# Kernel optimization log

Measured on AMD Instinct MI355X. Metric: run time of the kernel, lower is better.

Reference implementation:

```python
import jax, jax.numpy as jnp
import numpy as np

B, S, H = 1, 2048, 4096
NH = 32
NOPE, ROPE, VD = 128, 64, 128
QHD = NOPE + ROPE          # 192
QLR, KVLR = 1536, 512
BASE = 10000.0
EPS = 1e-6
SCALE = QHD ** -0.5


def _rmsnorm(x, w):
    xf = x.astype(jnp.float32)
    var = jnp.mean(xf * xf, axis=-1, keepdims=True)
    return (w * (xf * jax.lax.rsqrt(var + EPS))).astype(x.dtype)


def _rope_tables(seq_len):
    inv_freq = 1.0 / (BASE ** (jnp.arange(0, ROPE, 2, dtype=jnp.float32) / ROPE))
    t = jnp.arange(seq_len, dtype=jnp.float32)
    freqs = jnp.outer(t, inv_freq)                     # [S, ROPE/2]
    emb = jnp.concatenate([freqs, freqs], axis=-1)     # [S, ROPE]
    return jnp.cos(emb), jnp.sin(emb)


def _rotate_half(x):
    d = x.shape[-1] // 2
    return jnp.concatenate([-x[..., d:], x[..., :d]], axis=-1)


def setup_inputs() -> dict:
    key = jax.random.key(0)
    ks = jax.random.split(key, 8)
    w = 0.02
    hidden_states = jax.random.normal(ks[0], (B, S, H), dtype=jnp.float32)
    # additive causal mask, 0 on/below diagonal, -1e9 above
    causal = jnp.tril(jnp.ones((S, S), dtype=bool))
    attention_mask = jnp.where(causal, 0.0, -1e9).astype(jnp.float32)[None, None]
    return {
        "hidden_states": hidden_states,
        "attention_mask": attention_mask,
        "Wqa": jax.random.normal(ks[1], (QLR, H), dtype=jnp.float32) * w,
        "qa_ln_w": jnp.ones((QLR,), dtype=jnp.float32),
        "Wqb": jax.random.normal(ks[2], (NH * QHD, QLR), dtype=jnp.float32) * w,
        "Wkva": jax.random.normal(ks[3], (KVLR + ROPE, H), dtype=jnp.float32) * w,
        "kva_ln_w": jnp.ones((KVLR,), dtype=jnp.float32),
        "Wkvb": jax.random.normal(ks[4], (NH * (NOPE + VD), KVLR), dtype=jnp.float32) * w,
        "Wo": jax.random.normal(ks[5], (H, NH * VD), dtype=jnp.float32) * w,
    }


def reference(hidden_states, attention_mask, Wqa, qa_ln_w, Wqb, Wkva, kva_ln_w, Wkvb, Wo):
    bsz, q_len, _ = hidden_states.shape
    # --- Q path: low-rank down-proj + RMSNorm + up-proj ---
    q = _rmsnorm(hidden_states @ Wqa.T, qa_ln_w) @ Wqb.T          # [B,S,NH*QHD]
    q = q.reshape(bsz, q_len, NH, QHD).transpose(0, 2, 1, 3)      # [B,NH,S,QHD]
    q_nope, q_pe = q[..., :NOPE], q[..., NOPE:]
    # --- KV path: shared low-rank compression + decoupled rope key ---
    ckv = hidden_states @ Wkva.T                                   # [B,S,KVLR+ROPE]
    compressed_kv, k_pe = ckv[..., :KVLR], ckv[..., KVLR:]
    k_pe = k_pe.reshape(bsz, q_len, 1, ROPE).transpose(0, 2, 1, 3)  # [B,1,S,ROPE]
    kv = _rmsnorm(compressed_kv, kva_ln_w) @ Wkvb.T                # [B,S,NH*(NOPE+VD)]
    kv = kv.reshape(bsz, q_len, NH, NOPE + VD).transpose(0, 2, 1, 3)
    k_nope, value_states = kv[..., :NOPE], kv[..., NOPE:]
    # --- RoPE on decoupled dims ---
    cos, sin = _rope_tables(q_len)                                 # [S,ROPE] broadcast over B,NH
    q_pe = q_pe * cos + _rotate_half(q_pe) * sin
    k_pe = k_pe * cos + _rotate_half(k_pe) * sin
    query_states = jnp.concatenate([q_nope, q_pe], axis=-1)        # [B,NH,S,QHD]
    key_states = jnp.concatenate(
        [k_nope, jnp.broadcast_to(k_pe, (bsz, NH, q_len, ROPE))], axis=-1)
    # --- SDPA ---
    attn = jnp.einsum('bhqd,bhkd->bhqk', query_states, key_states) * SCALE
    attn = attn + attention_mask
    attn = jax.nn.softmax(attn.astype(jnp.float32), axis=-1).astype(query_states.dtype)
    out = jnp.einsum('bhqk,bhkd->bhqd', attn, value_states)        # [B,NH,S,VD]
    out = out.transpose(0, 2, 1, 3).reshape(bsz, q_len, NH * VD)
    return out @ Wo.T
```

## Files before the change

kernel.cpp:

```cpp
#include <hip/hip_runtime.h>

typedef __bf16 bf16;
typedef __bf16 bf16x8 __attribute__((ext_vector_type(8)));
typedef __bf16 bf16x4 __attribute__((ext_vector_type(4)));
typedef float  f32x4  __attribute__((ext_vector_type(4)));

#define NH_    32
#define S_     2048
#define H_     4096
#define NOPE_  128
#define ROPE_  64
#define VD_    128
#define QHD_   192
#define QLR_   1536
#define KVLR_  512
#define QKVA_N 2176

#define MFMA16(a, b, c) __builtin_amdgcn_mfma_f32_16x16x32_bf16(a, b, c, 0, 0, 0)

__device__ __forceinline__ void async_lds16(void* lds, const void* g) {
  __builtin_amdgcn_global_load_lds(
      (const __attribute__((address_space(1))) void*)g,
      (__attribute__((address_space(3))) void*)lds,
      16, 0, 0);
}

#define CVN1 2097152LL
#define CVN2 1572864LL
#define CVN3 655360LL
#define CVN4 2359296LL
#define CVN5 1048576LL
#define CVN6 4194304LL
#define CVC1 (CVN1)
#define CVC2 (CVC1 + CVN2)
#define CVC3 (CVC2 + CVN3)
#define CVC4 (CVC3 + CVN4)
#define CVC5 (CVC4 + CVN5)
#define CVC6 (CVC5 + CVN6)

__device__ __forceinline__ void cv4(const float* __restrict__ s, bf16* __restrict__ d,
                                    long long i) {
  float4 v = ((const float4*)s)[i];
  bf16x4 o;
  o[0] = (bf16)v.x; o[1] = (bf16)v.y; o[2] = (bf16)v.z; o[3] = (bf16)v.w;
  ((bf16x4*)d)[i] = o;
}

__global__ __launch_bounds__(256) void convert_all_kernel(
    const float* __restrict__ hs, const float* __restrict__ Wqa,
    const float* __restrict__ Wkva, const float* __restrict__ Wqb,
    const float* __restrict__ Wkvb, const float* __restrict__ Wo,
    bf16* __restrict__ hidden_bf, bf16* __restrict__ qkva_w,
    bf16* __restrict__ Wqb_bf, bf16* __restrict__ Wkvb_bf,
    bf16* __restrict__ Wo_bf) {
  long long i = (long long)blockIdx.x * 256 + threadIdx.x;
  const long long stride = (long long)gridDim.x * 256;
  for (; i < CVC6; i += stride) {
    if (i < CVC1) {
      cv4(hs, hidden_bf, i);
    } else if (i < CVC2) {
      cv4(Wqa, qkva_w, i - CVC1);
    } else if (i < CVC3) {
      long long j = i - CVC2;
      long long r = j >> 10;
      bf16x4 o;
      if (r < 576) {
        float4 v = ((const float4*)Wkva)[j];
        o[0] = (bf16)v.x; o[1] = (bf16)v.y; o[2] = (bf16)v.z; o[3] = (bf16)v.w;
      } else {
        o[0] = o[1] = o[2] = o[3] = (bf16)0.f;
      }
      ((bf16x4*)(qkva_w + (size_t)QLR_ * H_))[j] = o;
    } else if (i < CVC4) {
      cv4(Wqb, Wqb_bf, i - CVC3);
    } else if (i < CVC5) {
      cv4(Wkvb, Wkvb_bf, i - CVC4);
    } else {
      cv4(Wo, Wo_bf, i - CVC5);
    }
  }
}

__global__ __launch_bounds__(256) void rope_tables_kernel(float* __restrict__ ct,
                                                          float* __restrict__ st) {
  int i = blockIdx.x * 256 + threadIdx.x;
  int t = i >> 5, f = i & 31;
  float inv = powf(10000.0f, -(float)f / 32.0f);
  float ang = (float)t * inv;
  ct[i] = cosf(ang);
  st[i] = sinf(ang);
}

__global__ __launch_bounds__(256) void rope_q_kernel(bf16* __restrict__ qb,
                                                     const float* __restrict__ ct,
                                                     const float* __restrict__ st) {
  int i = blockIdx.x * 256 + threadIdx.x;
  int t = i >> 10;
  int rem = i & 1023;
  int h = rem >> 5, j = rem & 31;
  size_t base = (size_t)t * (NH_ * QHD_) + h * QHD_ + NOPE_;
  float a = (float)qb[base + j], b = (float)qb[base + 32 + j];
  float c = ct[t * 32 + j], s = st[t * 32 + j];
  qb[base + j]      = (bf16)(a * c - b * s);
  qb[base + 32 + j] = (bf16)(b * c + a * s);
}

__global__ __launch_bounds__(256) void rope_k_kernel(const float* __restrict__ part,
                                                     const float* __restrict__ ct,
                                                     const float* __restrict__ st,
                                                     bf16* __restrict__ kpe,
                                                     long long pstr) {
  int i = blockIdx.x * 256 + threadIdx.x;
  int t = i >> 5, j = i & 31;
  size_t base = (size_t)t * QKVA_N + 2048;
  float a = part[base + j] + part[base + j + pstr];
  float b = part[base + 32 + j] + part[base + 32 + j + pstr];
  float c = ct[i], s = st[i];
  kpe[t * 64 + j]      = (bf16)(a * c - b * s);
  kpe[t * 64 + 32 + j] = (bf16)(b * c + a * s);
}

template <int NS>
__global__ __launch_bounds__(256) void rmsnorm_kernel(const float* __restrict__ x,
                                                      const float* __restrict__ wt,
                                                      bf16* __restrict__ y,
                                                      int cols, int ldx, long long pstr) {
  const int row = blockIdx.x;
  const float* xr = x + (size_t)row * ldx;
  float ss = 0.f;
  for (int i = threadIdx.x; i < cols; i += 256) {
    float v = xr[i];
    if (NS > 1) v += xr[i + pstr];
    ss += v * v;
  }
  __shared__ float red[4];
  for (int off = 32; off > 0; off >>= 1) ss += __shfl_down(ss, off);
  if ((threadIdx.x & 63) == 0) red[threadIdx.x >> 6] = ss;
  __syncthreads();
  float tot = red[0] + red[1] + red[2] + red[3];
  float rr = 1.0f / sqrtf(tot / (float)cols + 1e-6f);
  bf16* yr = y + (size_t)row * cols;
  for (int i = threadIdx.x; i < cols; i += 256) {
    float v = xr[i];
    if (NS > 1) v += xr[i + pstr];
    yr[i] = (bf16)(wt[i] * v * rr);
  }
}

template <typename OutT, bool VOUT = false, int NSPLIT = 1>
__global__ __launch_bounds__(256) void gemm_bt(const bf16* __restrict__ A,
                                               const bf16* __restrict__ B,
                                               OutT* __restrict__ C,
                                               bf16* __restrict__ vTout,
                                               int M, int N, int K) {
  __shared__ bf16 SM[2 * 128 * 64];
  bf16* As = SM;
  bf16* Bs = SM + 128 * 64;
  const int tid = threadIdx.x;
  const int lane = tid & 63;
  const int w = tid >> 6;
  const int wm = w >> 1, wn = w & 1;

  const int nwg = gridDim.x * gridDim.y;
  const int lin = blockIdx.y * gridDim.x + blockIdx.x;
  const int cpx = nwg >> 3;
  const int swz = (lin & 7) * cpx + (lin >> 3);
  const int bx = swz % gridDim.x, by = swz / gridDim.x;

  const int m0 = by * 128, n0 = bx * 128;
  const int r15 = lane & 15;
  const int kbase = (lane >> 4) * 8;

  const int klen = K / NSPLIT;
  const int koff = (NSPLIT > 1) ? (int)blockIdx.z * klen : 0;
  OutT* Cz = (NSPLIT > 1) ? C + (size_t)blockIdx.z * M * (size_t)N : C;

  f32x4 acc[4][4];
#pragma unroll
  for (int i = 0; i < 4; ++i)
#pragma unroll
    for (int j = 0; j < 4; ++j) acc[i][j] = (f32x4){0.f, 0.f, 0.f, 0.f};

  for (int k0 = koff; k0 < koff + klen; k0 += 64) {
    __syncthreads();
#pragma unroll
    for (int s = 0; s < 4; ++s) {
      int lrow = w * 32 + s * 8 + (lane >> 3);
      int sc = (lane & 7) ^ (lrow & 7);
      const bf16* ga = A + (size_t)(m0 + lrow) * K + k0 + sc * 8;
      const bf16* gb = B + (size_t)(n0 + lrow) * K + k0 + sc * 8;
      async_lds16((char*)As + w * 4096 + s * 1024, ga);
      async_lds16((char*)Bs + w * 4096 + s * 1024, gb);
    }
    __syncthreads();

#pragma unroll
    for (int kk = 0; kk < 2; ++kk) {
      bf16x8 af[4], bfr[4];
#pragma unroll
      for (int i = 0; i < 4; ++i) {
        int ar = wm * 64 + i * 16 + r15;
        int off = ar * 128 + (kk * 32 + kbase) * 2;
        off ^= (ar & 7) << 4;
        af[i] = *(const bf16x8*)((const char*)As + off);
      }
#pragma unroll
      for (int j = 0; j < 4; ++j) {
        int br = wn * 64 + j * 16 + r15;
        int off = br * 128 + (kk * 32 + kbase) * 2;
        off ^= (br & 7) << 4;
        bfr[j] = *(const bf16x8*)((const char*)Bs + off);
      }
#pragma unroll
      for (int i = 0; i < 4; ++i)
#pragma unroll
        for (int j = 0; j < 4; ++j)
          acc[i][j] = MFMA16(af[i], bfr[j], acc[i][j]);
    }
  }

  const int rq = lane >> 4;

  if constexpr (VOUT) {
    if (bx & 1) {
      const int hh = bx >> 1;
      __syncthreads();
      bf16* TB = SM;
#pragma unroll
      for (int i = 0; i < 4; ++i)
#pragma unroll
        for (int j = 0; j < 4; ++j) {
          int cl = wn * 64 + j * 16 + r15;
          int rw0 = wm * 64 + i * 16 + rq * 4;
          bf16x4 hv;
#pragma unroll
          for (int r = 0; r < 4; ++r) hv[r] = (bf16)acc[i][j][r];
          *(bf16x4*)&TB[cl * 128 + (rw0 ^ ((cl & 7) << 3))] = hv;
        }
      __syncthreads();
#pragma unroll
      for (int it = 0; it < 8; ++it) {
        int cid = tid + it * 256;
        int dd = cid >> 4, cc = cid & 15;
        bf16x8 v = *(const bf16x8*)&TB[dd * 128 + ((cc ^ (dd & 7)) * 8)];
        *(bf16x8*)(vTout + ((size_t)hh * 128 + dd) * (size_t)M + m0 + cc * 8) = v;
      }
      return;
    }
  }

#pragma unroll
  for (int i = 0; i < 4; ++i)
#pragma unroll
    for (int j = 0; j < 4; ++j)
#pragma unroll
      for (int r = 0; r < 4; ++r) {
        int row = m0 + wm * 64 + i * 16 + rq * 4 + r;
        int col = n0 + wn * 64 + j * 16 + r15;
        Cz[(size_t)row * N + col] = (OutT)acc[i][j][r];
      }
}

__global__ __launch_bounds__(256) void attn_fwd(const bf16* __restrict__ q,
                                                const bf16* __restrict__ kv,
                                                const bf16* __restrict__ vT,
                                                const bf16* __restrict__ kpe,
                                                bf16* __restrict__ out) {
  __shared__ bf16 KN[64][136];
  __shared__ bf16 KP[64][72];
  __shared__ bf16 VS[128 * 64];
  __shared__ bf16 PS[4][16][72];

  const int h = blockIdx.x;
  const int qt = (gridDim.y - 1) - blockIdx.y;
  const int q0 = qt * 64;
  const int tid = threadIdx.x;
  const int lane = tid & 63;
  const int w = tid >> 6;
  const int r15 = lane & 15;
  const int g = lane >> 4;
  const int kbase = g * 8;

  const float SCALE = 0.07216878364870322f;
  const float CS = SCALE * 1.4426950408889634f;
  const float RTH = 8.0f / SCALE;

  bf16x8 qf[6];
  {
    const size_t qrow = q0 + w * 16 + r15;
    const bf16* qp = q + qrow * (NH_ * QHD_) + h * QHD_;
#pragma unroll
    for (int c = 0; c < 6; ++c) qf[c] = *(const bf16x8*)(qp + c * 32 + kbase);
  }

  f32x4 o[9];
#pragma unroll
  for (int d = 0; d < 9; ++d) o[d] = (f32x4){0.f, 0.f, 0.f, 0.f};
  float m[4] = {-1e30f, -1e30f, -1e30f, -1e30f};
  bf16x8 vone;
#pragma unroll
  for (int j = 0; j < 8; ++j) vone[j] = (bf16)1.f;

  const int pr_r = tid >> 4, pr_c = tid & 15;
  const int kp_r = tid >> 2, kp_c = tid & 3;
  const int vd = w * 32 + (lane >> 3);
  const int vc = lane & 7;
  const int vp = vc ^ (vd & 7);
  bf16x8 pKN[4], pV[4], pKP[2];
  auto load_tile = [&](int k0) {
#pragma unroll
    for (int it = 0; it < 4; ++it) {
      pKN[it] = *(const bf16x8*)(kv + (size_t)(k0 + pr_r + it * 16) * (NH_ * 256) + h * 256 + pr_c * 8);
      pV[it]  = *(const bf16x8*)(vT + ((size_t)h * 128 + vd + it * 8) * (size_t)S_ + k0 + vc * 8);
    }
    pKP[0] = *(const bf16x8*)(kpe + (size_t)(k0 + kp_r) * 64 + kp_c * 16);
    pKP[1] = *(const bf16x8*)(kpe + (size_t)(k0 + kp_r) * 64 + kp_c * 16 + 8);
  };

  load_tile(0);

  for (int kt = 0; kt <= qt; ++kt) {
    const int k0 = kt * 64;
    __syncthreads();
#pragma unroll
    for (int it = 0; it < 4; ++it) {
      *(bf16x8*)&KN[pr_r + it * 16][pr_c * 8] = pKN[it];
      *(bf16x8*)((char*)VS + (vd + it * 8) * 128 + vp * 16) = pV[it];
    }
    *(bf16x8*)&KP[kp_r][kp_c * 16] = pKP[0];
    *(bf16x8*)&KP[kp_r][kp_c * 16 + 8] = pKP[1];
    __syncthreads();

    if (kt < qt) load_tile(k0 + 64);

    f32x4 s[4];
    __builtin_amdgcn_s_setprio(1);
#pragma unroll
    for (int ct = 0; ct < 4; ++ct) {
      f32x4 a = (f32x4){0.f, 0.f, 0.f, 0.f};
#pragma unroll
      for (int c = 0; c < 4; ++c) {
        bf16x8 b = *(const bf16x8*)&KN[ct * 16 + r15][c * 32 + kbase];
        a = MFMA16(qf[c], b, a);
      }
#pragma unroll
      for (int c = 0; c < 2; ++c) {
        bf16x8 b = *(const bf16x8*)&KP[ct * 16 + r15][c * 32 + kbase];
        a = MFMA16(qf[4 + c], b, a);
      }
      s[ct] = a;
    }
    __builtin_amdgcn_s_setprio(0);

    const int qrow0 = q0 + w * 16 + g * 4;
    if (kt == qt) {
#pragma unroll
      for (int ct = 0; ct < 4; ++ct)
#pragma unroll
        for (int r = 0; r < 4; ++r)
          if ((k0 + ct * 16 + r15) > (qrow0 + r)) s[ct][r] = -1e30f;
    }

    float lm[4];
#pragma unroll
    for (int r = 0; r < 4; ++r)
      lm[r] = fmaxf(fmaxf(s[0][r], s[1][r]), fmaxf(s[2][r], s[3][r]));
    bool over = (lm[0] > m[0] + RTH) || (lm[1] > m[1] + RTH) ||
                (lm[2] > m[2] + RTH) || (lm[3] > m[3] + RTH);
    if (__any(over)) {
#pragma unroll
      for (int r = 0; r < 4; ++r) {
        float v = lm[r];
        v = fmaxf(v, __shfl_xor(v, 1));
        v = fmaxf(v, __shfl_xor(v, 2));
        v = fmaxf(v, __shfl_xor(v, 4));
        v = fmaxf(v, __shfl_xor(v, 8));
        float mn = fmaxf(m[r], v);
        float sc = exp2f((m[r] - mn) * CS);
        m[r] = mn;
#pragma unroll
        for (int d = 0; d < 9; ++d) o[d][r] *= sc;
      }
    }
#pragma unroll
    for (int ct = 0; ct < 4; ++ct)
#pragma unroll
      for (int r = 0; r < 4; ++r)
        PS[w][g * 4 + r][ct * 16 + r15] = (bf16)exp2f((s[ct][r] - m[r]) * CS);

    __builtin_amdgcn_s_setprio(1);
#pragma unroll
    for (int kk = 0; kk < 2; ++kk) {
      bf16x8 pa = *(const bf16x8*)&PS[w][r15][kk * 32 + kbase];
      const int kcx = (kk * 4 + g) ^ (r15 & 7);
      o[8] = MFMA16(pa, vone, o[8]);
#pragma unroll
      for (int dt = 0; dt < 8; ++dt) {
        int d = dt * 16 + r15;
        bf16x8 vb = *(const bf16x8*)((const char*)VS + d * 128 + kcx * 16);
        o[dt] = MFMA16(pa, vb, o[dt]);
      }
    }
    __builtin_amdgcn_s_setprio(0);
  }

  float invl[4];
#pragma unroll
  for (int r = 0; r < 4; ++r) invl[r] = 1.0f / o[8][r];
#pragma unroll
  for (int dt = 0; dt < 8; ++dt)
#pragma unroll
    for (int r = 0; r < 4; ++r) {
      int row = q0 + w * 16 + g * 4 + r;
      out[(size_t)row * (NH_ * VD_) + h * VD_ + dt * 16 + r15] = (bf16)(o[dt][r] * invl[r]);
    }
}

extern "C" void kernel_launch(void* const* d_in, const int* in_sizes, int n_in,
                              void* d_out, int out_size, void* d_ws, size_t ws_size,
                              hipStream_t stream) {
  (void)in_sizes; (void)n_in; (void)out_size; (void)ws_size;
  const float* hs     = (const float*)d_in[0];
  const float* Wqa    = (const float*)d_in[2];
  const float* qa_ln  = (const float*)d_in[3];
  const float* Wqb    = (const float*)d_in[4];
  const float* Wkva   = (const float*)d_in[5];
  const float* kva_ln = (const float*)d_in[6];
  const float* Wkvb   = (const float*)d_in[7];
  const float* Wo     = (const float*)d_in[8];
  float* outp = (float*)d_out;

  char* W = (char*)d_ws;
  size_t off = 0;
  auto nxt = [&](size_t b) { size_t o = off; off += (b + 255) & ~(size_t)255; return o; };
  bf16*  hidden_bf = (bf16*)(W + nxt((size_t)S_ * H_ * 2));
  bf16*  qkva_w    = (bf16*)(W + nxt((size_t)QKVA_N * H_ * 2));
  bf16*  Wqb_bf    = (bf16*)(W + nxt((size_t)NH_ * QHD_ * QLR_ * 2));
  bf16*  Wkvb_bf   = (bf16*)(W + nxt((size_t)NH_ * 256 * KVLR_ * 2));
  bf16*  Wo_bf     = (bf16*)(W + nxt((size_t)H_ * NH_ * VD_ * 2));
  bf16*  qa_norm   = (bf16*)(W + nxt((size_t)S_ * QLR_ * 2));
  bf16*  ckv_norm  = (bf16*)(W + nxt((size_t)S_ * KVLR_ * 2));
  bf16*  kpe       = (bf16*)(W + nxt((size_t)S_ * ROPE_ * 2));
  float* cost      = (float*)(W + nxt((size_t)S_ * 32 * 4));
  float* sint      = (float*)(W + nxt((size_t)S_ * 32 * 4));
  size_t Roff = nxt((size_t)S_ * NH_ * QHD_ * 2 + (size_t)S_ * NH_ * 256 * 2 +
                    (size_t)NH_ * VD_ * S_ * 2 + (size_t)S_ * NH_ * VD_ * 2);
  bf16* q_bf     = (bf16*)(W + Roff);
  bf16* kv_bf    = (bf16*)(W + Roff + (size_t)S_ * NH_ * QHD_ * 2);
  bf16* vT       = (bf16*)(W + Roff + (size_t)S_ * NH_ * QHD_ * 2 + (size_t)S_ * NH_ * 256 * 2);
  bf16* attn_out = (bf16*)(W + Roff + (size_t)S_ * NH_ * QHD_ * 2 + (size_t)S_ * NH_ * 256 * 2 +
                           (size_t)NH_ * VD_ * S_ * 2);
  float* part    = (float*)(W + Roff);
  const long long PSTR = (long long)S_ * QKVA_N;

  convert_all_kernel<<<2048, 256, 0, stream>>>(hs, Wqa, Wkva, Wqb, Wkvb, Wo,
                                               hidden_bf, qkva_w, Wqb_bf, Wkvb_bf, Wo_bf);
  rope_tables_kernel<<<256, 256, 0, stream>>>(cost, sint);

  gemm_bt<float, false, 2><<<dim3(QKVA_N / 128, S_ / 128, 2), 256, 0, stream>>>(
      hidden_bf, qkva_w, part, nullptr, S_, QKVA_N, H_);

  rmsnorm_kernel<2><<<S_, 256, 0, stream>>>(part, qa_ln, qa_norm, QLR_, QKVA_N, PSTR);
  rmsnorm_kernel<2><<<S_, 256, 0, stream>>>(part + QLR_, kva_ln, ckv_norm, KVLR_, QKVA_N, PSTR);
  rope_k_kernel<<<256, 256, 0, stream>>>(part, cost, sint, kpe, PSTR);

  gemm_bt<bf16><<<dim3(NH_ * QHD_ / 128, S_ / 128), 256, 0, stream>>>(
      qa_norm, Wqb_bf, q_bf, nullptr, S_, NH_ * QHD_, QLR_);
  rope_q_kernel<<<8192, 256, 0, stream>>>(q_bf, cost, sint);

  gemm_bt<bf16, true><<<dim3(NH_ * 256 / 128, S_ / 128), 256, 0, stream>>>(
      ckv_norm, Wkvb_bf, kv_bf, vT, S_, NH_ * 256, KVLR_);

  attn_fwd<<<dim3(NH_, S_ / 64), 256, 0, stream>>>(q_bf, kv_bf, vT, kpe, attn_out);

  gemm_bt<float><<<dim3(H_ / 128, S_ / 128), 256, 0, stream>>>(
      attn_out, Wo_bf, outp, nullptr, S_, H_, H_);
}
```

Before: 383.9 us.

## Fuse rope tables, rmsnorms, k-rope and q-rope into neighbouring kernels

Folds the RoPE table computation into the conversion kernel, merges both RMSNorms and the k_pe rotation into one per-row kernel, and applies q RoPE in the Wqb GEMM epilogue on the rope column block. This removes four small kernel launches and the extra read/write pass over q_bf. The epilogue rope relies on each 64-column warp tile that satisfies the selector lining up with a head's 64 rope dims.

```diff
diff --git a/kernel.cpp b/kernel.cpp
--- a/kernel.cpp
+++ b/kernel.cpp
@@ -31,12 +31,14 @@
 #define CVN4 2359296LL
 #define CVN5 1048576LL
 #define CVN6 4194304LL
+#define CVN7 16384LL
 #define CVC1 (CVN1)
 #define CVC2 (CVC1 + CVN2)
 #define CVC3 (CVC2 + CVN3)
 #define CVC4 (CVC3 + CVN4)
 #define CVC5 (CVC4 + CVN5)
 #define CVC6 (CVC5 + CVN6)
+#define CVC7 (CVC6 + CVN7)
 
 __device__ __forceinline__ void cv4(const float* __restrict__ s, bf16* __restrict__ d,
                                     long long i) {
@@ -52,10 +54,10 @@
     const float* __restrict__ Wkvb, const float* __restrict__ Wo,
     bf16* __restrict__ hidden_bf, bf16* __restrict__ qkva_w,
     bf16* __restrict__ Wqb_bf, bf16* __restrict__ Wkvb_bf,
-    bf16* __restrict__ Wo_bf) {
+    bf16* __restrict__ Wo_bf, float* __restrict__ ct, float* __restrict__ st) {
   long long i = (long long)blockIdx.x * 256 + threadIdx.x;
   const long long stride = (long long)gridDim.x * 256;
-  for (; i < CVC6; i += stride) {
+  for (; i < CVC7; i += stride) {
     if (i < CVC1) {
       cv4(hs, hidden_bf, i);
     } else if (i < CVC2) {
@@ -75,83 +77,80 @@
       cv4(Wqb, Wqb_bf, i - CVC3);
     } else if (i < CVC5) {
       cv4(Wkvb, Wkvb_bf, i - CVC4);
+    } else if (i < CVC6) {
+      cv4(Wo, Wo_bf, i - CVC5);
     } else {
-      cv4(Wo, Wo_bf, i - CVC5);
-    }
-  }
-}
-
-__global__ __launch_bounds__(256) void rope_tables_kernel(float* __restrict__ ct,
-                                                          float* __restrict__ st) {
-  int i = blockIdx.x * 256 + threadIdx.x;
-  int t = i >> 5, f = i & 31;
-  float inv = powf(10000.0f, -(float)f / 32.0f);
-  float ang = (float)t * inv;
-  ct[i] = cosf(ang);
-  st[i] = sinf(ang);
-}
-
-__global__ __launch_bounds__(256) void rope_q_kernel(bf16* __restrict__ qb,
-                                                     const float* __restrict__ ct,
-                                                     const float* __restrict__ st) {
-  int i = blockIdx.x * 256 + threadIdx.x;
-  int t = i >> 10;
-  int rem = i & 1023;
-  int h = rem >> 5, j = rem & 31;
-  size_t base = (size_t)t * (NH_ * QHD_) + h * QHD_ + NOPE_;
-  float a = (float)qb[base + j], b = (float)qb[base + 32 + j];
-  float c = ct[t * 32 + j], s = st[t * 32 + j];
-  qb[base + j]      = (bf16)(a * c - b * s);
-  qb[base + 32 + j] = (bf16)(b * c + a * s);
-}
-
-__global__ __launch_bounds__(256) void rope_k_kernel(const float* __restrict__ part,
-                                                     const float* __restrict__ ct,
-                                                     const float* __restrict__ st,
-                                                     bf16* __restrict__ kpe,
-                                                     long long pstr) {
-  int i = blockIdx.x * 256 + threadIdx.x;
-  int t = i >> 5, j = i & 31;
-  size_t base = (size_t)t * QKVA_N + 2048;
-  float a = part[base + j] + part[base + j + pstr];
-  float b = part[base + 32 + j] + part[base + 32 + j + pstr];
-  float c = ct[i], s = st[i];
-  kpe[t * 64 + j]      = (bf16)(a * c - b * s);
-  kpe[t * 64 + 32 + j] = (bf16)(b * c + a * s);
-}
-
-template <int NS>
-__global__ __launch_bounds__(256) void rmsnorm_kernel(const float* __restrict__ x,
-                                                      const float* __restrict__ wt,
-                                                      bf16* __restrict__ y,
-                                                      int cols, int ldx, long long pstr) {
+      long long j4 = (i - CVC6) * 4;
+#pragma unroll
+      for (int k = 0; k < 4; ++k) {
+        long long idx = j4 + k;
+        int t = (int)(idx >> 5), f = (int)(idx & 31);
+        float inv = powf(10000.0f, -(float)f / 32.0f);
+        float ang = (float)t * inv;
+        ct[idx] = cosf(ang);
+        st[idx] = sinf(ang);
+      }
+    }
+  }
+}
+
+__global__ __launch_bounds__(256) void norm_rope_kernel(
+    const float* __restrict__ part, const float* __restrict__ qa_ln,
+    const float* __restrict__ kva_ln, bf16* __restrict__ qa_norm,
+    bf16* __restrict__ ckv_norm, bf16* __restrict__ kpe,
+    const float* __restrict__ ct, const float* __restrict__ st, long long pstr) {
   const int row = blockIdx.x;
-  const float* xr = x + (size_t)row * ldx;
-  float ss = 0.f;
-  for (int i = threadIdx.x; i < cols; i += 256) {
-    float v = xr[i];
-    if (NS > 1) v += xr[i + pstr];
-    ss += v * v;
-  }
-  __shared__ float red[4];
-  for (int off = 32; off > 0; off >>= 1) ss += __shfl_down(ss, off);
-  if ((threadIdx.x & 63) == 0) red[threadIdx.x >> 6] = ss;
+  const int tid = threadIdx.x;
+  const float* xr = part + (size_t)row * QKVA_N;
+  float ssq = 0.f, ssk = 0.f;
+#pragma unroll
+  for (int it = 0; it < 6; ++it) {
+    float v = xr[tid + it * 256] + xr[tid + it * 256 + pstr];
+    ssq += v * v;
+  }
+#pragma unroll
+  for (int it = 6; it < 8; ++it) {
+    float v = xr[tid + it * 256] + xr[tid + it * 256 + pstr];
+    ssk += v * v;
+  }
+  __shared__ float redq[4], redk[4];
+  for (int o = 32; o > 0; o >>= 1) {
+    ssq += __shfl_down(ssq, o);
+    ssk += __shfl_down(ssk, o);
+  }
+  if ((tid & 63) == 0) { redq[tid >> 6] = ssq; redk[tid >> 6] = ssk; }
   __syncthreads();
-  float tot = red[0] + red[1] + red[2] + red[3];
-  float rr = 1.0f / sqrtf(tot / (float)cols + 1e-6f);
-  bf16* yr = y + (size_t)row * cols;
-  for (int i = threadIdx.x; i < cols; i += 256) {
-    float v = xr[i];
-    if (NS > 1) v += xr[i + pstr];
-    yr[i] = (bf16)(wt[i] * v * rr);
-  }
-}
-
-template <typename OutT, bool VOUT = false, int NSPLIT = 1>
+  float rq = 1.0f / sqrtf((redq[0] + redq[1] + redq[2] + redq[3]) / (float)QLR_ + 1e-6f);
+  float rk = 1.0f / sqrtf((redk[0] + redk[1] + redk[2] + redk[3]) / (float)KVLR_ + 1e-6f);
+#pragma unroll
+  for (int it = 0; it < 6; ++it) {
+    int i = tid + it * 256;
+    float v = xr[i] + xr[i + pstr];
+    qa_norm[(size_t)row * QLR_ + i] = (bf16)(qa_ln[i] * v * rq);
+  }
+#pragma unroll
+  for (int it = 6; it < 8; ++it) {
+    int i = tid + it * 256;
+    float v = xr[i] + xr[i + pstr];
+    ckv_norm[(size_t)row * KVLR_ + (i - 1536)] = (bf16)(kva_ln[i - 1536] * v * rk);
+  }
+  if (tid < 32) {
+    int j = tid;
+    float a = xr[2048 + j] + xr[2048 + j + pstr];
+    float b = xr[2048 + 32 + j] + xr[2048 + 32 + j + pstr];
+    float c = ct[row * 32 + j], s = st[row * 32 + j];
+    kpe[row * 64 + j]      = (bf16)(a * c - b * s);
+    kpe[row * 64 + 32 + j] = (bf16)(b * c + a * s);
+  }
+}
+
+template <typename OutT, bool VOUT = false, int NSPLIT = 1, bool QROPE = false>
 __global__ __launch_bounds__(256) void gemm_bt(const bf16* __restrict__ A,
                                                const bf16* __restrict__ B,
                                                OutT* __restrict__ C,
                                                bf16* __restrict__ vTout,
+                                               const float* __restrict__ ct,
+                                               const float* __restrict__ st,
                                                int M, int N, int K) {
   __shared__ bf16 SM[2 * 128 * 64];
   bf16* As = SM;
@@ -246,6 +245,25 @@
         *(bf16x8*)(vTout + ((size_t)hh * 128 + dd) * (size_t)M + m0 + cc * 8) = v;
       }
       return;
+    }
+  }
+
+  if constexpr (QROPE) {
+    if (((bx << 1) + wn) % 3 == 2) {
+#pragma unroll
+      for (int i = 0; i < 4; ++i)
+#pragma unroll
+        for (int r = 0; r < 4; ++r) {
+          int t = m0 + wm * 64 + i * 16 + rq * 4 + r;
+#pragma unroll
+          for (int jf = 0; jf < 2; ++jf) {
+            int j = jf * 16 + r15;
+            float c = ct[t * 32 + j], s = st[t * 32 + j];
+            float a = acc[i][jf][r], b = acc[i][jf + 2][r];
+            acc[i][jf][r]     = a * c - b * s;
+            acc[i][jf + 2][r] = b * c + a * s;
+          }
+        }
     }
   }
 
@@ -454,25 +472,23 @@
   const long long PSTR = (long long)S_ * QKVA_N;
 
   convert_all_kernel<<<2048, 256, 0, stream>>>(hs, Wqa, Wkva, Wqb, Wkvb, Wo,
-                                               hidden_bf, qkva_w, Wqb_bf, Wkvb_bf, Wo_bf);
-  rope_tables_kernel<<<256, 256, 0, stream>>>(cost, sint);
+                                               hidden_bf, qkva_w, Wqb_bf, Wkvb_bf, Wo_bf,
+                                               cost, sint);
 
   gemm_bt<float, false, 2><<<dim3(QKVA_N / 128, S_ / 128, 2), 256, 0, stream>>>(
-      hidden_bf, qkva_w, part, nullptr, S_, QKVA_N, H_);
-
-  rmsnorm_kernel<2><<<S_, 256, 0, stream>>>(part, qa_ln, qa_norm, QLR_, QKVA_N, PSTR);
-  rmsnorm_kernel<2><<<S_, 256, 0, stream>>>(part + QLR_, kva_ln, ckv_norm, KVLR_, QKVA_N, PSTR);
-  rope_k_kernel<<<256, 256, 0, stream>>>(part, cost, sint, kpe, PSTR);
-
-  gemm_bt<bf16><<<dim3(NH_ * QHD_ / 128, S_ / 128), 256, 0, stream>>>(
-      qa_norm, Wqb_bf, q_bf, nullptr, S_, NH_ * QHD_, QLR_);
-  rope_q_kernel<<<8192, 256, 0, stream>>>(q_bf, cost, sint);
+      hidden_bf, qkva_w, part, nullptr, nullptr, nullptr, S_, QKVA_N, H_);
+
+  norm_rope_kernel<<<S_, 256, 0, stream>>>(part, qa_ln, kva_ln, qa_norm, ckv_norm,
+                                           kpe, cost, sint, PSTR);
+
+  gemm_bt<bf16, false, 1, true><<<dim3(NH_ * QHD_ / 128, S_ / 128), 256, 0, stream>>>(
+      qa_norm, Wqb_bf, q_bf, nullptr, cost, sint, S_, NH_ * QHD_, QLR_);
 
   gemm_bt<bf16, true><<<dim3(NH_ * 256 / 128, S_ / 128), 256, 0, stream>>>(
-      ckv_norm, Wkvb_bf, kv_bf, vT, S_, NH_ * 256, KVLR_);
+      ckv_norm, Wkvb_bf, kv_bf, vT, nullptr, nullptr, S_, NH_ * 256, KVLR_);
 
   attn_fwd<<<dim3(NH_, S_ / 64), 256, 0, stream>>>(q_bf, kv_bf, vT, kpe, attn_out);
 
   gemm_bt<float><<<dim3(H_ / 128, S_ / 128), 256, 0, stream>>>(
-      attn_out, Wo_bf, outp, nullptr, S_, H_, H_);
-}
+      attn_out, Wo_bf, outp, nullptr, nullptr, nullptr, S_, H_, H_);
+}
```

After: 396.2 us. 3.2% more time.
